# Optimization experiments

Hardware: AMD Instinct MI355X
Metric: run time of the kernel (lower is better)

Reference implementation:

```python
import jax, jax.numpy as jnp
import numpy as np

NUM_CLASSES = 32
MAX_DET = 100        # max_detections
CONF = 0.25          # conf_threshold
IOU_THR = 0.45       # iou_threshold
BATCH = 64
ANCHORS = 8400


def setup_inputs() -> dict:
    key = jax.random.key(0)
    # raw YOLO head output [B, 4+num_classes, anchors]; uniform [0,1) so boxes
    # (normalized cx,cy,w,h) and class scores are in valid range.
    yolo_output = jax.random.uniform(key, (BATCH, 4 + NUM_CLASSES, ANCHORS), dtype=jnp.float32)
    return {"yolo_output": yolo_output}


def _iou_one_vs_all(box, boxes):
    # box: [4] (ymin,xmin,ymax,xmax); boxes: [A,4]
    y1 = jnp.maximum(box[0], boxes[:, 0])
    x1 = jnp.maximum(box[1], boxes[:, 1])
    y2 = jnp.minimum(box[2], boxes[:, 2])
    x2 = jnp.minimum(box[3], boxes[:, 3])
    inter = jnp.maximum(y2 - y1, 0.0) * jnp.maximum(x2 - x1, 0.0)
    area_a = (box[2] - box[0]) * (box[3] - box[1])
    area_b = (boxes[:, 2] - boxes[:, 0]) * (boxes[:, 3] - boxes[:, 1])
    union = area_a + area_b - inter
    return jnp.where(union > 0.0, inter / union, 0.0)


def _nms_one_image(boxes, classes, scores):
    # Greedy hard NMS, equivalent to tf.image.non_max_suppression followed by
    # gather + zero-pad to MAX_DET. `scores` already has sub-threshold anchors
    # masked to -1 (emulating boolean_mask by threshold).
    def step(sc, _):
        idx = jnp.argmax(sc)
        s = sc[idx]
        b = boxes[idx]
        c = classes[idx]
        ok = s > 0.0  # any remaining valid candidate?
        iou = _iou_one_vs_all(b, boxes)
        new_sc = jnp.where(iou > IOU_THR, -1.0, sc).at[idx].set(-1.0)
        sc = jnp.where(ok, new_sc, sc)
        out = (jnp.where(ok, b, 0.0), jnp.where(ok, c, 0.0), jnp.where(ok, s, 0.0), ok)
        return sc, out

    _, (sel_boxes, sel_classes, sel_scores, valid) = jax.lax.scan(
        step, scores, None, length=MAX_DET)
    num_det = jnp.sum(valid.astype(jnp.float32))
    return sel_boxes, sel_classes, sel_scores, num_det


def _forward(yolo_output):
    # [B, 36, A] -> [B, A, 36]
    t = jnp.transpose(yolo_output, (0, 2, 1))
    boxes_raw = t[..., :4]                      # cx, cy, w, h (normalized)
    class_scores = t[..., 4:]                   # [B, A, num_classes]
    best_scores = jnp.max(class_scores, axis=-1)
    best_classes = jax.lax.stop_gradient(
        jnp.argmax(class_scores, axis=-1).astype(jnp.float32))
    xc, yc, w, h = (boxes_raw[..., 0], boxes_raw[..., 1],
                    boxes_raw[..., 2], boxes_raw[..., 3])
    clip = lambda v: jnp.clip(v, 0.0, 1.0)
    # TF order: [ymin, xmin, ymax, xmax]
    corner = jnp.stack([clip(yc - h * 0.5), clip(xc - w * 0.5),
                        clip(yc + h * 0.5), clip(xc + w * 0.5)], axis=-1)
    # confidence threshold: mask out instead of boolean_mask (jit-friendly)
    masked_scores = jnp.where(best_scores >= CONF, best_scores, -1.0)
    det_boxes, det_classes, det_scores, num_det = jax.vmap(_nms_one_image)(
        corner, best_classes, masked_scores)
    return det_boxes, det_classes, det_scores, num_det


def reference(yolo_output):
    # Returns (detection_boxes [B,100,4], detection_classes [B,100],
    #          detection_scores [B,100], num_detections [B])
    return _forward(yolo_output)
```

## Files before the change

### kernel.cpp

```cpp
#include <hip/hip_runtime.h>

#define BATCH   64
#define CHANS   36
#define ANCH    8400
#define NCLS    32
#define MAXDET  100
#define CONF    0.25f
#define KTOP    512
#define NBUCK   2048
#define BUCK0   (0x3E800000u >> 13)
#define STPB    512
#define SNW     (STPB / 64)
#define SNLD    17

typedef unsigned long long u64;
typedef unsigned int       u32;

__device__ __forceinline__ bool iou_gt(float ay1, float ax1, float ay2, float ax2, float aar,
                                       float by1, float bx1, float by2, float bx2, float bar,
                                       double M) {
#pragma clang fp contract(off)
    float iy1 = fmaxf(ay1, by1), ix1 = fmaxf(ax1, bx1);
    float iy2 = fminf(ay2, by2), ix2 = fminf(ax2, bx2);
    float inter = fmaxf(iy2 - iy1, 0.f) * fmaxf(ix2 - ix1, 0.f);
    float uni = (aar + bar) - inter;
    return (double)inter > M * (double)uni;
}

__global__ __launch_bounds__(256) void yolo_prep(const float* __restrict__ in,
                                                 float4* __restrict__ wbox,
                                                 u64* __restrict__ wk64) {
#pragma clang fp contract(off)
    const int G2 = ANCH / 2;
    int g = blockIdx.x * 256 + threadIdx.x;
    if (g >= G2) return;
    int b = blockIdx.y;
    const float2* p = (const float2*)(in + (size_t)b * (CHANS * ANCH));
    float2 xc = p[0 * G2 + g], yc = p[1 * G2 + g], ww = p[2 * G2 + g], hh = p[3 * G2 + g];
    float2 best = p[4 * G2 + g];
    uint2 bc = make_uint2(0, 0);
#pragma unroll
    for (int k = 1; k < NCLS; ++k) {
        float2 v = p[(4 + k) * G2 + g];
        if (v.x > best.x) { best.x = v.x; bc.x = k; }
        if (v.y > best.y) { best.y = v.y; bc.y = k; }
    }
    int a0 = b * ANCH + 2 * g;
    u64* wk = wk64 + (size_t)b * ANCH + 2 * g;
#define PREP_C(C, I)                                                      \
    {                                                                     \
        float Y1 = fminf(fmaxf(yc.C - hh.C * 0.5f, 0.f), 1.f);            \
        float X1 = fminf(fmaxf(xc.C - ww.C * 0.5f, 0.f), 1.f);            \
        float Y2 = fminf(fmaxf(yc.C + hh.C * 0.5f, 0.f), 1.f);            \
        float X2 = fminf(fmaxf(xc.C + ww.C * 0.5f, 0.f), 1.f);            \
        wbox[a0 + I] = make_float4(Y1, X1, Y2, X2);                       \
        int a_ = 2 * g + I;                                               \
        wk[I] = (best.C >= CONF)                                          \
            ? (((u64)__float_as_uint(best.C) << 32) |                     \
               ((u64)(16383 - a_) << 18) | (u64)(bc.C & 31u))             \
            : 0ull;                                                       \
    }
    PREP_C(x, 0) PREP_C(y, 1)
#undef PREP_C
}

__global__ __launch_bounds__(STPB) void yolo_sort(u64* __restrict__ wk64,
                                                  u32* __restrict__ meta) {
    int b = blockIdx.x, t = threadIdx.x;
    u64* gk = wk64 + (size_t)b * ANCH;

    __shared__ u32 hist[NBUCK];
    __shared__ u32 wvcnt[SNW];
    __shared__ u32 kred[SNW];

    for (int i = t; i < NBUCK; i += STPB) hist[i] = 0u;
    __syncthreads();

    u64 kk[SNLD];
#pragma unroll
    for (int j = 0; j < SNLD; ++j) {
        int a = t + j * STPB;
        u64 k = (a < ANCH) ? gk[a] : 0ull;
        kk[j] = k;
        if (k != 0ull) atomicAdd(&hist[(int)((u32)(k >> 45) - BUCK0)], 1u);
    }
    __syncthreads();

    int u0 = t * 4;
    u32 c0 = hist[2047 - u0], c1 = hist[2047 - (u0 + 1)],
        c2 = hist[2047 - (u0 + 2)], c3 = hist[2047 - (u0 + 3)];
    u32 l1 = c0 + c1, l2 = l1 + c2, Su = l2 + c3;
    u32 x = Su;
#pragma unroll
    for (int d = 1; d < 64; d <<= 1) {
        u32 y = __shfl_up(x, d, 64);
        if ((t & 63) >= d) x += y;
    }
    if ((t & 63) == 63) wvcnt[t >> 6] = x;
    __syncthreads();
    int wb = 0;
    for (int w = 0; w < (t >> 6); ++w) wb += (int)wvcnt[w];
    int T = 0;
    for (int w = 0; w < SNW; ++w) T += (int)wvcnt[w];
    u32 excl = (u32)wb + x - Su;
    hist[u0]     = excl;
    hist[u0 + 1] = excl + c0;
    hist[u0 + 2] = excl + l1;
    hist[u0 + 3] = excl + l2;
    __syncthreads();

#pragma unroll
    for (int j = 0; j < SNLD; ++j) {
        if (kk[j] != 0ull) {
            int r = 2047 - (int)((u32)(kk[j] >> 45) - BUCK0);
            u32 pos = atomicAdd(&hist[r], 1u);
            gk[pos] = kk[j];
        }
    }
    __syncthreads();

    u32 kb = 0;
#pragma unroll
    for (int q = 0; q < 4; ++q) {
        u32 v = hist[u0 + q];
        if (v <= (u32)KTOP && v > kb) kb = v;
    }
#pragma unroll
    for (int sh = 1; sh < 64; sh <<= 1) {
        u32 o = __shfl_xor(kb, sh, 64);
        if (o > kb) kb = o;
    }
    if ((t & 63) == 0) kred[t >> 6] = kb;
    __syncthreads();
    if (t == 0) {
        u32 K = 0;
        for (int w = 0; w < SNW; ++w) if (kred[w] > K) K = kred[w];
        meta[b * 4 + 0] = K;
        meta[b * 4 + 1] = (u32)T;
    }
}

__global__ __launch_bounds__(256) void yolo_matrix(const float4* __restrict__ wbox,
                                                   const u64* __restrict__ wk64,
                                                   const u32* __restrict__ meta,
                                                   u64* __restrict__ gS) {
#pragma clang fp contract(off)
    const double M = (double)0.45f + 0x1p-26;
    int b = blockIdx.x, t = threadIdx.x;
    const float4* bx = wbox + (size_t)b * ANCH;
    const u64* gk = wk64 + (size_t)b * ANCH;
    int K = (int)meta[b * 4 + 0];

    __shared__ u64    ck[KTOP];
    __shared__ float4 cb[KTOP];
    __shared__ float  ca[KTOP];

    for (int i = t; i < KTOP; i += 256) {
        u64 k = (i < K) ? gk[i] : 0ull;
        ck[i] = k;
        float4 bb = make_float4(0.f, 0.f, 0.f, 0.f);
        if (k != 0ull) {
            int a = 16383 - (int)((k >> 18) & 0x3FFFull);
            bb = bx[a];
        }
        cb[i] = bb;
        ca[i] = (bb.z - bb.x) * (bb.w - bb.y);
    }
    __syncthreads();

    int row = blockIdx.y * 64 + (t >> 2);
    int seg = t & 3;
    u64 kr = ck[row];
    float4 rb = cb[row];
    float rar = ca[row];
    u64 w0 = 0ull, w1 = 0ull;
    int base0 = seg * 128;
#pragma unroll 4
    for (int j = 0; j < 64; ++j) {
        {
            int i = base0 + j;
            u64 ki = ck[i];
            if ((ki > kr) && iou_gt(cb[i].x, cb[i].y, cb[i].z, cb[i].w, ca[i],
                                    rb.x, rb.y, rb.z, rb.w, rar, M))
                w0 |= 1ull << j;
        }
        {
            int i = base0 + 64 + j;
            u64 ki = ck[i];
            if ((ki > kr) && iou_gt(cb[i].x, cb[i].y, cb[i].z, cb[i].w, ca[i],
                                    rb.x, rb.y, rb.z, rb.w, rar, M))
                w1 |= 1ull << j;
        }
    }
    ulonglong2 wv; wv.x = w0; wv.y = w1;
    *(ulonglong2*)&gS[(size_t)b * (KTOP * 8) + (size_t)row * 8 + seg * 2] = wv;
}

__global__ __launch_bounds__(256) void yolo_resolve(const float4* __restrict__ wbox,
                                                    u64* __restrict__ wk64,
                                                    const u64* __restrict__ gS,
                                                    const u32* __restrict__ meta,
                                                    float* __restrict__ out) {
#pragma clang fp contract(off)
    const double M = (double)0.45f + 0x1p-26;
    int b = blockIdx.x, t = threadIdx.x;
    const float4* bx = wbox + (size_t)b * ANCH;
    u64* gk = wk64 + (size_t)b * ANCH;
    int K = (int)meta[b * 4 + 0], T = (int)meta[b * 4 + 1];

    __shared__ u64   ck[KTOP];
    __shared__ u64   SP[KTOP * 9];
    __shared__ u64   selKey[KTOP];
    __shared__ float selb[MAXDET][5];
    __shared__ u64   redm[4];
    __shared__ int   selTotS;

    float* outBox = out + (size_t)b * (MAXDET * 4);
    float* outCls = out + (size_t)(BATCH * MAXDET * 4) + b * MAXDET;
    float* outScr = out + (size_t)(BATCH * MAXDET * 5) + b * MAXDET;
    float* outNum = out + (size_t)(BATCH * MAXDET * 6) + b;

    for (int i = t; i < KTOP; i += 256) ck[i] = (i < K) ? gk[i] : 0ull;
    const u64* gSb = gS + (size_t)b * (KTOP * 8);
    for (int i = t; i < KTOP * 8; i += 256) SP[(i >> 3) * 9 + (i & 7)] = gSb[i];
    __syncthreads();

    u64 S[8];
#pragma unroll
    for (int w = 0; w < 8; ++w) S[w] = 0ull;
    if (t < 64) {
        int L = t;
        u64 U[8];
#pragma unroll
        for (int w = 0; w < 8; ++w) U[w] = __ballot(ck[(w << 6) + L] != 0ull);
        for (int it = 0; it < KTOP; ++it) {
            if (!(U[0] | U[1] | U[2] | U[3] | U[4] | U[5] | U[6] | U[7])) break;
            u64 D[8];
#pragma unroll
            for (int w = 0; w < 8; ++w) {
                const u64* rm = &SP[((w << 6) + L) * 9];
                u64 pend = (rm[0] & U[0]) | (rm[1] & U[1]) | (rm[2] & U[2]) | (rm[3] & U[3])
                         | (rm[4] & U[4]) | (rm[5] & U[5]) | (rm[6] & U[6]) | (rm[7] & U[7]);
                D[w] = __ballot(((U[w] >> L) & 1ull) && (pend == 0ull));
            }
#pragma unroll
            for (int w = 0; w < 8; ++w) { S[w] |= D[w]; U[w] &= ~D[w]; }
#pragma unroll
            for (int w = 0; w < 8; ++w) {
                const u64* rm = &SP[((w << 6) + L) * 9];
                u64 hit = (rm[0] & D[0]) | (rm[1] & D[1]) | (rm[2] & D[2]) | (rm[3] & D[3])
                        | (rm[4] & D[4]) | (rm[5] & D[5]) | (rm[6] & D[6]) | (rm[7] & D[7]);
                U[w] &= ~__ballot(((U[w] >> L) & 1ull) && (hit != 0ull));
            }
        }
        if (t == 0) {
            int c = 0;
#pragma unroll
            for (int w = 0; w < 8; ++w) c += (int)__popcll(S[w]);
            selTotS = c;
        }
    }
    __syncthreads();

    if (t < 64) {
        int L = t, base = 0;
#pragma unroll
        for (int w = 0; w < 8; ++w) {
            u64 Sw = S[w];
            if ((Sw >> L) & 1ull) {
                int r = base + (int)__popcll(Sw & ((1ull << L) - 1ull));
                selKey[r] = ck[(w << 6) + L];
            }
            base += (int)__popcll(Sw);
        }
    }
    __syncthreads();

    int sTot = selTotS;
    int s = sTot < MAXDET ? sTot : MAXDET;

    if (t < 64) {
        int L = t;
#pragma unroll
        for (int w = 0; w < 8; ++w) {
            if ((S[w] >> L) & 1ull) {
                u64 myk = ck[(w << 6) + L];
                int pos = 0;
                for (int j = 0; j < sTot; ++j) pos += (selKey[j] > myk) ? 1 : 0;
                if (pos < MAXDET) {
                    int a = 16383 - (int)((myk >> 18) & 0x3FFFull);
                    float4 bb = bx[a];
                    outScr[pos] = __uint_as_float((u32)(myk >> 32));
                    outCls[pos] = (float)((u32)myk & 31u);
                    outBox[pos * 4 + 0] = bb.x; outBox[pos * 4 + 1] = bb.y;
                    outBox[pos * 4 + 2] = bb.z; outBox[pos * 4 + 3] = bb.w;
                    selb[pos][0] = bb.x; selb[pos][1] = bb.y; selb[pos][2] = bb.z;
                    selb[pos][3] = bb.w; selb[pos][4] = (bb.z - bb.x) * (bb.w - bb.y);
                }
            }
        }
    }
    __syncthreads();

    if (s < MAXDET && T > K) {
        int NR = T - K;
        u64* rk = gk + K;
        for (int i = t; i < NR; i += 256) {
            u64 k = rk[i];
            if (!k) continue;
            int a = 16383 - (int)((k >> 18) & 0x3FFFull);
            float4 bb = bx[a];
            float ar = (bb.z - bb.x) * (bb.w - bb.y);
            for (int j = 0; j < s; ++j) {
                if (iou_gt(selb[j][0], selb[j][1], selb[j][2], selb[j][3], selb[j][4],
                           bb.x, bb.y, bb.z, bb.w, ar, M)) { rk[i] = 0ull; break; }
            }
        }
        __syncthreads();
        while (s < MAXDET) {
            u64 best = 0ull;
            for (int i = t; i < NR; i += 256) { u64 k = rk[i]; if (k > best) best = k; }
#pragma unroll
            for (int sh = 1; sh < 64; sh <<= 1) {
                u64 o = __shfl_xor(best, sh, 64);
                if (o > best) best = o;
            }
            if ((t & 63) == 0) redm[t >> 6] = best;
            __syncthreads();
            best = redm[0];
            for (int w = 1; w < 4; ++w) if (redm[w] > best) best = redm[w];
            if (best == 0ull) break;
            int a = 16383 - (int)((best >> 18) & 0x3FFFull);
            float4 nb = bx[a];
            float nar = (nb.z - nb.x) * (nb.w - nb.y);
            if (t == 0) {
                outScr[s] = __uint_as_float((u32)(best >> 32));
                outCls[s] = (float)((u32)best & 31u);
                outBox[s * 4 + 0] = nb.x; outBox[s * 4 + 1] = nb.y;
                outBox[s * 4 + 2] = nb.z; outBox[s * 4 + 3] = nb.w;
            }
            for (int i = t; i < NR; i += 256) {
                u64 k = rk[i];
                if (k != 0ull) {
                    if (k == best) rk[i] = 0ull;
                    else {
                        int a2 = 16383 - (int)((k >> 18) & 0x3FFFull);
                        float4 bb = bx[a2];
                        float ar = (bb.z - bb.x) * (bb.w - bb.y);
                        if (iou_gt(nb.x, nb.y, nb.z, nb.w, nar,
                                   bb.x, bb.y, bb.z, bb.w, ar, M)) rk[i] = 0ull;
                    }
                }
            }
            ++s;
            __syncthreads();
        }
    }

    for (int q = s + t; q < MAXDET; q += 256) {
        outScr[q] = 0.f; outCls[q] = 0.f;
        outBox[q * 4 + 0] = 0.f; outBox[q * 4 + 1] = 0.f;
        outBox[q * 4 + 2] = 0.f; outBox[q * 4 + 3] = 0.f;
    }
    if (t == 0) *outNum = (float)s;
}

extern "C" void kernel_launch(void* const* d_in, const int* in_sizes, int n_in,
                              void* d_out, int out_size, void* d_ws, size_t ws_size,
                              hipStream_t stream) {
    const float* in = (const float*)d_in[0];
    float* out = (float*)d_out;
    float4* wbox = (float4*)d_ws;
    u64*    wk64 = (u64*)((char*)d_ws + (size_t)BATCH * ANCH * 16);
    u64*    gS   = (u64*)((char*)d_ws + (size_t)BATCH * ANCH * 24);
    u32*    meta = (u32*)((char*)d_ws + (size_t)BATCH * ANCH * 24 + (size_t)BATCH * KTOP * 64);

    dim3 gp((ANCH / 2 + 255) / 256, BATCH);
    yolo_prep<<<gp, 256, 0, stream>>>(in, wbox, wk64);
    yolo_sort<<<BATCH, STPB, 0, stream>>>(wk64, meta);
    yolo_matrix<<<dim3(BATCH, 8), 256, 0, stream>>>(wbox, wk64, meta, gS);
    yolo_resolve<<<BATCH, 256, 0, stream>>>(wbox, wk64, gS, meta, out);
}
```

Before: 175.6 us.

## Fuse histogram into prep and replace full bucket sort with threshold partition

The prep kernel now handles four anchors per thread with float4 loads. It also builds the per-image score histogram in shared memory and flushes it to a global histogram with atomics. The full counting-sort scatter kernel is replaced by a lighter kernel that scans the histogram to find the bucket threshold giving at most KTOP candidates, then compacts those keys into a small buffer with an atomic counter. The candidate buffer is therefore unsorted. The fallback greedy loop now scans all anchors and drops the already-handled top buckets on the fly. This removes the sort pass but adds a memset, global atomics, and full-array scans in the fallback path.

```diff
diff --git a/kernel.cpp b/kernel.cpp
--- a/kernel.cpp
+++ b/kernel.cpp
@@ -9,9 +9,6 @@
 #define KTOP    512
 #define NBUCK   2048
 #define BUCK0   (0x3E800000u >> 13)
-#define STPB    512
-#define SNW     (STPB / 64)
-#define SNLD    17
 
 typedef unsigned long long u64;
 typedef unsigned int       u32;
@@ -29,126 +26,144 @@
 
 __global__ __launch_bounds__(256) void yolo_prep(const float* __restrict__ in,
                                                  float4* __restrict__ wbox,
-                                                 u64* __restrict__ wk64) {
+                                                 u64* __restrict__ wk64,
+                                                 u32* __restrict__ hist) {
 #pragma clang fp contract(off)
-    const int G2 = ANCH / 2;
+    const int G = ANCH / 4;
     int g = blockIdx.x * 256 + threadIdx.x;
-    if (g >= G2) return;
     int b = blockIdx.y;
-    const float2* p = (const float2*)(in + (size_t)b * (CHANS * ANCH));
-    float2 xc = p[0 * G2 + g], yc = p[1 * G2 + g], ww = p[2 * G2 + g], hh = p[3 * G2 + g];
-    float2 best = p[4 * G2 + g];
-    uint2 bc = make_uint2(0, 0);
-#pragma unroll
-    for (int k = 1; k < NCLS; ++k) {
-        float2 v = p[(4 + k) * G2 + g];
-        if (v.x > best.x) { best.x = v.x; bc.x = k; }
-        if (v.y > best.y) { best.y = v.y; bc.y = k; }
-    }
-    int a0 = b * ANCH + 2 * g;
-    u64* wk = wk64 + (size_t)b * ANCH + 2 * g;
-#define PREP_C(C, I)                                                      \
-    {                                                                     \
-        float Y1 = fminf(fmaxf(yc.C - hh.C * 0.5f, 0.f), 1.f);            \
-        float X1 = fminf(fmaxf(xc.C - ww.C * 0.5f, 0.f), 1.f);            \
-        float Y2 = fminf(fmaxf(yc.C + hh.C * 0.5f, 0.f), 1.f);            \
-        float X2 = fminf(fmaxf(xc.C + ww.C * 0.5f, 0.f), 1.f);            \
-        wbox[a0 + I] = make_float4(Y1, X1, Y2, X2);                       \
-        int a_ = 2 * g + I;                                               \
-        wk[I] = (best.C >= CONF)                                          \
-            ? (((u64)__float_as_uint(best.C) << 32) |                     \
-               ((u64)(16383 - a_) << 18) | (u64)(bc.C & 31u))             \
-            : 0ull;                                                       \
-    }
-    PREP_C(x, 0) PREP_C(y, 1)
+    bool act = (g < G);
+
+    __shared__ u32 lh[NBUCK];
+    for (int i = threadIdx.x; i < NBUCK; i += 256) lh[i] = 0u;
+    __syncthreads();
+
+    if (act) {
+        const float4* p = (const float4*)(in + (size_t)b * (CHANS * ANCH));
+        float4 xc = p[0 * G + g], yc = p[1 * G + g], ww = p[2 * G + g], hh = p[3 * G + g];
+        float4 best = p[4 * G + g];
+        uint4 bc = make_uint4(0, 0, 0, 0);
+#pragma unroll
+        for (int k = 1; k < NCLS; ++k) {
+            float4 v = p[(4 + k) * G + g];
+            if (v.x > best.x) { best.x = v.x; bc.x = k; }
+            if (v.y > best.y) { best.y = v.y; bc.y = k; }
+            if (v.z > best.z) { best.z = v.z; bc.z = k; }
+            if (v.w > best.w) { best.w = v.w; bc.w = k; }
+        }
+        int a0 = b * ANCH + 4 * g;
+        u64* wk = wk64 + (size_t)b * ANCH + 4 * g;
+#define PREP_C(C, I)                                                          \
+        {                                                                     \
+            float Y1 = fminf(fmaxf(yc.C - hh.C * 0.5f, 0.f), 1.f);            \
+            float X1 = fminf(fmaxf(xc.C - ww.C * 0.5f, 0.f), 1.f);            \
+            float Y2 = fminf(fmaxf(yc.C + hh.C * 0.5f, 0.f), 1.f);            \
+            float X2 = fminf(fmaxf(xc.C + ww.C * 0.5f, 0.f), 1.f);            \
+            wbox[a0 + I] = make_float4(Y1, X1, Y2, X2);                       \
+            u64 kv = 0ull;                                                    \
+            if (best.C >= CONF) {                                             \
+                u32 sb = __float_as_uint(best.C);                             \
+                kv = ((u64)sb << 32) |                                        \
+                     ((u64)(16383 - (4 * g + I)) << 18) | (u64)(bc.C & 31u);  \
+                atomicAdd(&lh[(sb >> 13) - BUCK0], 1u);                       \
+            }                                                                 \
+            wk[I] = kv;                                                       \
+        }
+        PREP_C(x, 0) PREP_C(y, 1) PREP_C(z, 2) PREP_C(w, 3)
 #undef PREP_C
-}
-
-__global__ __launch_bounds__(STPB) void yolo_sort(u64* __restrict__ wk64,
-                                                  u32* __restrict__ meta) {
+    }
+    __syncthreads();
+    u32* gh = hist + (size_t)b * NBUCK;
+    for (int i = threadIdx.x; i < NBUCK; i += 256) {
+        u32 c = lh[i];
+        if (c) atomicAdd(&gh[i], c);
+    }
+}
+
+__global__ __launch_bounds__(256) void yolo_taupart(u64* __restrict__ wk64,
+                                                    const u32* __restrict__ hist,
+                                                    u64* __restrict__ gkA,
+                                                    u32* __restrict__ meta) {
     int b = blockIdx.x, t = threadIdx.x;
-    u64* gk = wk64 + (size_t)b * ANCH;
-
-    __shared__ u32 hist[NBUCK];
-    __shared__ u32 wvcnt[SNW];
-    __shared__ u32 kred[SNW];
-
-    for (int i = t; i < NBUCK; i += STPB) hist[i] = 0u;
-    __syncthreads();
-
-    u64 kk[SNLD];
-#pragma unroll
-    for (int j = 0; j < SNLD; ++j) {
-        int a = t + j * STPB;
-        u64 k = (a < ANCH) ? gk[a] : 0ull;
-        kk[j] = k;
-        if (k != 0ull) atomicAdd(&hist[(int)((u32)(k >> 45) - BUCK0)], 1u);
-    }
-    __syncthreads();
-
-    int u0 = t * 4;
-    u32 c0 = hist[2047 - u0], c1 = hist[2047 - (u0 + 1)],
-        c2 = hist[2047 - (u0 + 2)], c3 = hist[2047 - (u0 + 3)];
-    u32 l1 = c0 + c1, l2 = l1 + c2, Su = l2 + c3;
+    const u32* gh = hist + (size_t)b * NBUCK;
+
+    __shared__ u32 wsum[4];
+    __shared__ u32 bestP;
+    __shared__ u32 shT;
+    __shared__ u32 curA;
+    __shared__ u32 staub;
+    if (t == 0) { bestP = 0u; curA = 0u; }
+    __syncthreads();
+
+    u32 c[8], sloc[8];
+    u32 run = 0;
+#pragma unroll
+    for (int q = 0; q < 8; ++q) {
+        int r = t * 8 + q;
+        c[q] = gh[2047 - r];
+        run += c[q];
+        sloc[q] = run;
+    }
+    u32 Su = run;
     u32 x = Su;
 #pragma unroll
     for (int d = 1; d < 64; d <<= 1) {
         u32 y = __shfl_up(x, d, 64);
         if ((t & 63) >= d) x += y;
     }
-    if ((t & 63) == 63) wvcnt[t >> 6] = x;
-    __syncthreads();
-    int wb = 0;
-    for (int w = 0; w < (t >> 6); ++w) wb += (int)wvcnt[w];
-    int T = 0;
-    for (int w = 0; w < SNW; ++w) T += (int)wvcnt[w];
-    u32 excl = (u32)wb + x - Su;
-    hist[u0]     = excl;
-    hist[u0 + 1] = excl + c0;
-    hist[u0 + 2] = excl + l1;
-    hist[u0 + 3] = excl + l2;
-    __syncthreads();
-
-#pragma unroll
-    for (int j = 0; j < SNLD; ++j) {
-        if (kk[j] != 0ull) {
-            int r = 2047 - (int)((u32)(kk[j] >> 45) - BUCK0);
-            u32 pos = atomicAdd(&hist[r], 1u);
-            gk[pos] = kk[j];
-        }
-    }
-    __syncthreads();
-
-    u32 kb = 0;
-#pragma unroll
-    for (int q = 0; q < 4; ++q) {
-        u32 v = hist[u0 + q];
-        if (v <= (u32)KTOP && v > kb) kb = v;
-    }
-#pragma unroll
-    for (int sh = 1; sh < 64; sh <<= 1) {
-        u32 o = __shfl_xor(kb, sh, 64);
-        if (o > kb) kb = o;
-    }
-    if ((t & 63) == 0) kred[t >> 6] = kb;
+    if ((t & 63) == 63) wsum[t >> 6] = x;
+    __syncthreads();
+    u32 base = 0;
+    for (int w = 0; w < (t >> 6); ++w) base += wsum[w];
+    u32 excl = base + x - Su;
+
+    u32 mypk = 0;
+#pragma unroll
+    for (int q = 0; q < 8; ++q) {
+        u32 inc = excl + sloc[q];
+        if (inc <= (u32)KTOP) {
+            u32 pk = (inc << 11) | (u32)(t * 8 + q);
+            if (pk > mypk) mypk = pk;
+        }
+    }
+    if (mypk) atomicMax(&bestP, mypk);
+    if (t == 255) shT = excl + Su;
     __syncthreads();
     if (t == 0) {
-        u32 K = 0;
-        for (int w = 0; w < SNW; ++w) if (kred[w] > K) K = kred[w];
+        u32 bp = bestP, K, taub;
+        if (bp == 0u) { K = 0u; taub = (u32)NBUCK; }
+        else { K = bp >> 11; taub = 2047u - (bp & 0x7FFu); }
         meta[b * 4 + 0] = K;
-        meta[b * 4 + 1] = (u32)T;
+        meta[b * 4 + 1] = shT;
+        meta[b * 4 + 2] = taub;
+        staub = taub;
+    }
+    __syncthreads();
+    u32 taub = staub;
+
+    const u64* gk = wk64 + (size_t)b * ANCH;
+    u64* ga = gkA + (size_t)b * KTOP;
+    for (int j = 0; j < 33; ++j) {
+        int a = t + j * 256;
+        if (a < ANCH) {
+            u64 k = gk[a];
+            if (k != 0ull && ((u32)(k >> 45) - BUCK0) >= taub) {
+                u32 slot = atomicAdd(&curA, 1u);
+                ga[slot] = k;
+            }
+        }
     }
 }
 
 __global__ __launch_bounds__(256) void yolo_matrix(const float4* __restrict__ wbox,
-                                                   const u64* __restrict__ wk64,
+                                                   const u64* __restrict__ gkA,
                                                    const u32* __restrict__ meta,
                                                    u64* __restrict__ gS) {
 #pragma clang fp contract(off)
     const double M = (double)0.45f + 0x1p-26;
     int b = blockIdx.x, t = threadIdx.x;
     const float4* bx = wbox + (size_t)b * ANCH;
-    const u64* gk = wk64 + (size_t)b * ANCH;
+    const u64* ga = gkA + (size_t)b * KTOP;
     int K = (int)meta[b * 4 + 0];
 
     __shared__ u64    ck[KTOP];
@@ -156,7 +171,7 @@
     __shared__ float  ca[KTOP];
 
     for (int i = t; i < KTOP; i += 256) {
-        u64 k = (i < K) ? gk[i] : 0ull;
+        u64 k = (i < K) ? ga[i] : 0ull;
         ck[i] = k;
         float4 bb = make_float4(0.f, 0.f, 0.f, 0.f);
         if (k != 0ull) {
@@ -198,6 +213,7 @@
 
 __global__ __launch_bounds__(256) void yolo_resolve(const float4* __restrict__ wbox,
                                                     u64* __restrict__ wk64,
+                                                    const u64* __restrict__ gkA,
                                                     const u64* __restrict__ gS,
                                                     const u32* __restrict__ meta,
                                                     float* __restrict__ out) {
@@ -206,7 +222,9 @@
     int b = blockIdx.x, t = threadIdx.x;
     const float4* bx = wbox + (size_t)b * ANCH;
     u64* gk = wk64 + (size_t)b * ANCH;
+    const u64* ga = gkA + (size_t)b * KTOP;
     int K = (int)meta[b * 4 + 0], T = (int)meta[b * 4 + 1];
+    u32 taub = meta[b * 4 + 2];
 
     __shared__ u64   ck[KTOP];
     __shared__ u64   SP[KTOP * 9];
@@ -220,7 +238,7 @@
     float* outScr = out + (size_t)(BATCH * MAXDET * 5) + b * MAXDET;
     float* outNum = out + (size_t)(BATCH * MAXDET * 6) + b;
 
-    for (int i = t; i < KTOP; i += 256) ck[i] = (i < K) ? gk[i] : 0ull;
+    for (int i = t; i < KTOP; i += 256) ck[i] = (i < K) ? ga[i] : 0ull;
     const u64* gSb = gS + (size_t)b * (KTOP * 8);
     for (int i = t; i < KTOP * 8; i += 256) SP[(i >> 3) * 9 + (i & 7)] = gSb[i];
     __syncthreads();
@@ -303,23 +321,23 @@
     __syncthreads();
 
     if (s < MAXDET && T > K) {
-        int NR = T - K;
-        u64* rk = gk + K;
-        for (int i = t; i < NR; i += 256) {
-            u64 k = rk[i];
-            if (!k) continue;
-            int a = 16383 - (int)((k >> 18) & 0x3FFFull);
-            float4 bb = bx[a];
-            float ar = (bb.z - bb.x) * (bb.w - bb.y);
-            for (int j = 0; j < s; ++j) {
-                if (iou_gt(selb[j][0], selb[j][1], selb[j][2], selb[j][3], selb[j][4],
-                           bb.x, bb.y, bb.z, bb.w, ar, M)) { rk[i] = 0ull; break; }
+        for (int i = t; i < ANCH; i += 256) {
+            u64 k = gk[i];
+            if (k != 0ull) {
+                if (((u32)(k >> 45) - BUCK0) >= taub) { gk[i] = 0ull; continue; }
+                int a = 16383 - (int)((k >> 18) & 0x3FFFull);
+                float4 bb = bx[a];
+                float ar = (bb.z - bb.x) * (bb.w - bb.y);
+                for (int j = 0; j < s; ++j) {
+                    if (iou_gt(selb[j][0], selb[j][1], selb[j][2], selb[j][3], selb[j][4],
+                               bb.x, bb.y, bb.z, bb.w, ar, M)) { gk[i] = 0ull; break; }
+                }
             }
         }
         __syncthreads();
         while (s < MAXDET) {
             u64 best = 0ull;
-            for (int i = t; i < NR; i += 256) { u64 k = rk[i]; if (k > best) best = k; }
+            for (int i = t; i < ANCH; i += 256) { u64 k = gk[i]; if (k > best) best = k; }
 #pragma unroll
             for (int sh = 1; sh < 64; sh <<= 1) {
                 u64 o = __shfl_xor(best, sh, 64);
@@ -339,16 +357,16 @@
                 outBox[s * 4 + 0] = nb.x; outBox[s * 4 + 1] = nb.y;
                 outBox[s * 4 + 2] = nb.z; outBox[s * 4 + 3] = nb.w;
             }
-            for (int i = t; i < NR; i += 256) {
-                u64 k = rk[i];
+            for (int i = t; i < ANCH; i += 256) {
+                u64 k = gk[i];
                 if (k != 0ull) {
-                    if (k == best) rk[i] = 0ull;
+                    if (k == best) gk[i] = 0ull;
                     else {
                         int a2 = 16383 - (int)((k >> 18) & 0x3FFFull);
                         float4 bb = bx[a2];
                         float ar = (bb.z - bb.x) * (bb.w - bb.y);
                         if (iou_gt(nb.x, nb.y, nb.z, nb.w, nar,
-                                   bb.x, bb.y, bb.z, bb.w, ar, M)) rk[i] = 0ull;
+                                   bb.x, bb.y, bb.z, bb.w, ar, M)) gk[i] = 0ull;
                     }
                 }
             }
@@ -370,14 +388,18 @@
                               hipStream_t stream) {
     const float* in = (const float*)d_in[0];
     float* out = (float*)d_out;
-    float4* wbox = (float4*)d_ws;
-    u64*    wk64 = (u64*)((char*)d_ws + (size_t)BATCH * ANCH * 16);
-    u64*    gS   = (u64*)((char*)d_ws + (size_t)BATCH * ANCH * 24);
-    u32*    meta = (u32*)((char*)d_ws + (size_t)BATCH * ANCH * 24 + (size_t)BATCH * KTOP * 64);
-
-    dim3 gp((ANCH / 2 + 255) / 256, BATCH);
-    yolo_prep<<<gp, 256, 0, stream>>>(in, wbox, wk64);
-    yolo_sort<<<BATCH, STPB, 0, stream>>>(wk64, meta);
-    yolo_matrix<<<dim3(BATCH, 8), 256, 0, stream>>>(wbox, wk64, meta, gS);
-    yolo_resolve<<<BATCH, 256, 0, stream>>>(wbox, wk64, gS, meta, out);
-}
+    char* w = (char*)d_ws;
+    float4* wbox = (float4*)w;
+    u64*    wk64 = (u64*)(w + 8601600);
+    u64*    gkA  = (u64*)(w + 8601600 + 4300800);
+    u64*    gS   = (u64*)(w + 8601600 + 4300800 + 262144);
+    u32*    hist = (u32*)(w + 8601600 + 4300800 + 262144 + 2097152);
+    u32*    meta = (u32*)(w + 8601600 + 4300800 + 262144 + 2097152 + 524288);
+
+    hipMemsetAsync(hist, 0, (size_t)BATCH * NBUCK * 4, stream);
+    dim3 gp((ANCH / 4 + 255) / 256, BATCH);
+    yolo_prep<<<gp, 256, 0, stream>>>(in, wbox, wk64, hist);
+    yolo_taupart<<<BATCH, 256, 0, stream>>>(wk64, hist, gkA, meta);
+    yolo_matrix<<<dim3(BATCH, 8), 256, 0, stream>>>(wbox, gkA, meta, gS);
+    yolo_resolve<<<BATCH, 256, 0, stream>>>(wbox, wk64, gkA, gS, meta, out);
+}
```

Result: slower. 184.3 us (+5.0%).
